# Optimization experiments

Hardware: AMD Instinct MI355X
Metric: run time of the kernel (lower is better)

## Reference

```python
import jax, jax.numpy as jnp
import numpy as np

N, T, F, HID, HEADS, E = 10000, 6, 64, 64, 4, 160000


def gat_conv(x, W, a_src, a_dst, bias, src, dst, n, concat):
    """PyG-style GATConv (self-loops already appended to src/dst).
    x: [n, in]; W: [in, H*C]; a_src/a_dst: [H, C]; returns ([n, H*C] or [n, C], alpha [E', H])."""
    H, C = a_src.shape
    xw = (x @ W).reshape(n, H, C)
    # per-edge unnormalized attention logits
    al = (xw * a_src).sum(-1)[src] + (xw * a_dst).sum(-1)[dst]  # [E', H]
    al = jax.nn.leaky_relu(al, 0.2)
    # segment softmax over destination neighborhoods
    m = jax.ops.segment_max(al, dst, num_segments=n)
    ex = jnp.exp(al - m[dst])
    s = jax.ops.segment_sum(ex, dst, num_segments=n)
    alpha = ex / (s[dst] + 1e-16)
    out = jax.ops.segment_sum(xw[src] * alpha[:, :, None], dst, num_segments=n)  # [n, H, C]
    out = out.reshape(n, H * C) if concat else out.mean(axis=1)
    return out + bias, alpha


def setup_inputs() -> dict:
    key = jax.random.key(0)
    ks = jax.random.split(key, 12)
    sc = 0.05
    return {
        "x": jax.random.normal(ks[0], (N, T, F), jnp.float32),
        "edge_index": jax.random.randint(ks[1], (2, E), 0, N, jnp.int64),
        "W0": jax.random.normal(ks[2], (F, HID), jnp.float32) * sc,
        "a_src0": jax.random.normal(ks[3], (HEADS, HID // HEADS), jnp.float32) * sc,
        "a_dst0": jax.random.normal(ks[4], (HEADS, HID // HEADS), jnp.float32) * sc,
        "b0": jnp.zeros((HID,), jnp.float32),
        "W1": jax.random.normal(ks[5], (HID, HEADS * HID), jnp.float32) * sc,
        "a_src1": jax.random.normal(ks[6], (HEADS, HID), jnp.float32) * sc,
        "a_dst1": jax.random.normal(ks[7], (HEADS, HID), jnp.float32) * sc,
        "b1": jnp.zeros((HID,), jnp.float32),
        "ln_g": jnp.ones((HID,), jnp.float32),
        "ln_b": jnp.zeros((HID,), jnp.float32),
        "W_ih": jax.random.normal(ks[8], (3 * HID, HID), jnp.float32) * sc,
        "W_hh": jax.random.normal(ks[9], (3 * HID, HID), jnp.float32) * sc,
        "b_ih": jnp.zeros((3 * HID,), jnp.float32),
        "b_hh": jnp.zeros((3 * HID,), jnp.float32),
    }


def reference(x, edge_index, W0, a_src0, a_dst0, b0, W1, a_src1, a_dst1, b1,
              ln_g, ln_b, W_ih, W_hh, b_ih, b_hh):
    n = x.shape[0]
    loops = jnp.arange(n)
    src = jnp.concatenate([edge_index[0], loops])  # add self loops
    dst = jnp.concatenate([edge_index[1], loops])

    def gat_step(_, xt):
        h, _a = gat_conv(xt, W0, a_src0, a_dst0, b0, src, dst, n, True)
        h = jax.nn.elu(h)  # dropout is identity in eval mode
        h, alpha = gat_conv(h, W1, a_src1, a_dst1, b1, src, dst, n, False)
        h = jax.nn.elu(h)
        mu = h.mean(-1, keepdims=True)
        v = ((h - mu) ** 2).mean(-1, keepdims=True)
        h = (h - mu) / jnp.sqrt(v + 1e-5) * ln_g + ln_b
        return None, (h, alpha)

    _, (Hs, alphas) = jax.lax.scan(gat_step, None, jnp.moveaxis(x, 1, 0))  # Hs: [T, n, HID]

    def gru_step(h, xt):
        gi = xt @ W_ih.T + b_ih
        gh = h @ W_hh.T + b_hh
        ir, iz, ig = jnp.split(gi, 3, axis=-1)
        hr, hz, hg = jnp.split(gh, 3, axis=-1)
        r = jax.nn.sigmoid(ir + hr)
        z = jax.nn.sigmoid(iz + hz)
        g = jnp.tanh(ig + r * hg)
        return (1.0 - z) * g + z * h, None

    h0 = jnp.zeros((n, W_hh.shape[1]), x.dtype)
    hT, _ = jax.lax.scan(gru_step, h0, Hs)  # last GRU output == last hidden (1 layer)
    attn_edge_index = jnp.stack([src, dst])
    return hT, alphas[-1], attn_edge_index
```

## Files before the change

kernel.cpp:

```cpp
#include <hip/hip_runtime.h>
#include <hip/hip_bf16.h>
#include <cstdint>
#include <cstddef>

#define N_NODES 10000
#define T_STEPS 6
#define F_IN    64
#define HID     64
#define HEADS   4
#define E_EDGES 160000
#define EP      (E_EDGES + N_NODES)
#define TN      (T_STEPS * N_NODES)
#define NTILES  (TN / 16)
#define CAP     96

typedef __hip_bfloat16 bf16;
typedef __attribute__((ext_vector_type(8))) short short8;
typedef __attribute__((ext_vector_type(4))) float floatx4;

__device__ __forceinline__ float bfu(unsigned short s) { return __uint_as_float((unsigned)s << 16); }
__device__ __forceinline__ unsigned short f2bu(float f) {
    bf16 b = __float2bfloat16(f);
    return *(unsigned short*)&b;
}
__device__ __forceinline__ void lds_fence() {
    asm volatile("s_waitcnt lgkmcnt(0)" ::: "memory");
}
__device__ __forceinline__ int xcd_swizzle(int b, int nblk) {
    int q = nblk >> 3, r = nblk & 7;
    int x = b & 7, j = b >> 3;
    return (x < r ? x * (q + 1) : r * (q + 1) + (x - r) * q) + j;
}


__global__ void k_scatter(const int* ei, int* fill,
                          int* csr_src, int* csr_eid, float* out_ei) {
    int e = blockIdx.x * blockDim.x + threadIdx.x;
    if (e >= EP) return;
    int src = (e < E_EDGES) ? ei[e] : (e - E_EDGES);
    int dst = (e < E_EDGES) ? ei[E_EDGES + e] : (e - E_EDGES);
    int pos = atomicAdd(&fill[dst], 1);
    if (pos < CAP) {
        csr_src[dst * CAP + pos] = src;
        csr_eid[dst * CAP + pos] = e;
    }
    out_ei[e] = (float)src;
    out_ei[EP + e] = (float)dst;
}


__global__ __launch_bounds__(256) void k_prep(const float* __restrict__ W0,
                                              const float* __restrict__ W1,
                                              const float* __restrict__ a_src0,
                                              const float* __restrict__ a_dst0,
                                              const float* __restrict__ a_src1,
                                              const float* __restrict__ a_dst1,
                                              const float* __restrict__ W_ih,
                                              const float* __restrict__ W_hh,
                                              bf16* __restrict__ W0bt,
                                              bf16* __restrict__ W1bt,
                                              bf16* __restrict__ wihb,
                                              bf16* __restrict__ whhb,
                                              float* __restrict__ P0s,
                                              float* __restrict__ P0d,
                                              float* __restrict__ P1s,
                                              float* __restrict__ P1d) {
    int b = blockIdx.x, tid = threadIdx.x;
    if (b == 176) {
        int h = tid >> 6, k = tid & 63;
        float ps = 0.f, pd = 0.f;
        for (int c = 0; c < 64; c++) {
            float wv = W1[k * 256 + h * 64 + c];
            ps += wv * a_src1[h * 64 + c];
            pd += wv * a_dst1[h * 64 + c];
        }
        P1s[h * 64 + k] = ps;
        P1d[h * 64 + k] = pd;
        return;
    }
    if (b == 177) {
        int h = tid >> 6, k = tid & 63;
        float ps = 0.f, pd = 0.f;
        for (int c = 0; c < 16; c++) {
            float wv = W0[k * 64 + h * 16 + c];
            ps += wv * a_src0[h * 16 + c];
            pd += wv * a_dst0[h * 16 + c];
        }
        P0s[h * 64 + k] = ps;
        P0d[h * 64 + k] = pd;
        return;
    }
    int i = b * 256 + tid;
    if (i < 4096) {
        W0bt[i] = __float2bfloat16(W0[(i & 63) * 64 + (i >> 6)]);
    } else if (i < 20480) {
        int j = i - 4096; int c = j >> 8, K = j & 255;
        W1bt[j] = __float2bfloat16(W1[(K & 63) * 256 + (K >> 6) * 64 + c]);
    } else if (i < 32768) {
        wihb[i - 20480] = __float2bfloat16(W_ih[i - 20480]);
    } else {
        whhb[i - 32768] = __float2bfloat16(W_hh[i - 32768]);
    }
}

__global__ __launch_bounds__(256) void k_gemm0(const float* __restrict__ x,
                                               const bf16* __restrict__ W0bt,
                                               const float* __restrict__ P0s,
                                               const float* __restrict__ P0d,
                                               bf16* __restrict__ XW0b,
                                               float* __restrict__ ALS0,
                                               float* __restrict__ ALD0) {
    __shared__ __align__(16) bf16 wt[64 * 64];
    int tid = threadIdx.x;
    for (int i = tid; i < 512; i += 256)
        ((short8*)wt)[i] = ((const short8*)W0bt)[i];
    __syncthreads();
    int wv = tid >> 6, lane = tid & 63;
    int tile = blockIdx.x * 4 + wv;
    if (tile >= NTILES) return;
    int rb = tile * 16;
    int m = lane & 15, quad = lane >> 4;
    int row = rb + m;
    int t = row / N_NODES, n = row - t * N_NODES;
    const float* xr = x + ((size_t)n * T_STEPS + t) * F_IN + quad * 8;
    short8 a0, a1;
#pragma unroll
    for (int j = 0; j < 8; j++) {
        a0[j] = (short)f2bu(xr[j]);
        a1[j] = (short)f2bu(xr[32 + j]);
    }
    floatx4 acc[4];
#pragma unroll
    for (int ct = 0; ct < 4; ct++) {
        short8 bb0 = *(const short8*)(wt + (ct * 16 + m) * 64 + quad * 8);
        short8 bb1 = *(const short8*)(wt + (ct * 16 + m) * 64 + 32 + quad * 8);
        floatx4 a = {0.f, 0.f, 0.f, 0.f};
        a = __builtin_amdgcn_mfma_f32_16x16x32_bf16(a0, bb0, a, 0, 0, 0);
        a = __builtin_amdgcn_mfma_f32_16x16x32_bf16(a1, bb1, a, 0, 0, 0);
        acc[ct] = a;
    }
    short8 p0, p1;
#pragma unroll
    for (int j = 0; j < 8; j++) {
        int k0 = quad * 8 + j, k1 = 32 + quad * 8 + j;
        float v0 = 0.f, v1 = 0.f;
        if (m < 4)      { v0 = P0s[m * 64 + k0];       v1 = P0s[m * 64 + k1]; }
        else if (m < 8) { v0 = P0d[(m - 4) * 64 + k0]; v1 = P0d[(m - 4) * 64 + k1]; }
        p0[j] = (short)f2bu(v0);
        p1[j] = (short)f2bu(v1);
    }
    floatx4 ac5 = {0.f, 0.f, 0.f, 0.f};
    ac5 = __builtin_amdgcn_mfma_f32_16x16x32_bf16(a0, p0, ac5, 0, 0, 0);
    ac5 = __builtin_amdgcn_mfma_f32_16x16x32_bf16(a1, p1, ac5, 0, 0, 0);
#pragma unroll
    for (int ct = 0; ct < 4; ct++)
#pragma unroll
        for (int r = 0; r < 4; r++)
            XW0b[(size_t)(rb + quad * 4 + r) * 64 + ct * 16 + m] = __float2bfloat16(acc[ct][r]);
#pragma unroll
    for (int r = 0; r < 4; r++) {
        int orow = rb + quad * 4 + r;
        if (m < 4)      ALS0[orow * 4 + m] = ac5[r];
        else if (m < 8) ALD0[orow * 4 + (m - 4)] = ac5[r];
    }
}

__global__ __launch_bounds__(256) void k_fused0(const int* __restrict__ fill,
                                                const int* __restrict__ csr_src,
                                                const bf16* __restrict__ XW0b,
                                                const float* __restrict__ ALS0,
                                                const float* __restrict__ ALD0,
                                                const float* __restrict__ b0,
                                                const float* __restrict__ P1s,
                                                const float* __restrict__ P1d,
                                                bf16* __restrict__ H0b,
                                                float* __restrict__ ALS1,
                                                float* __restrict__ ALD1) {
    __shared__ unsigned short srcs[4][4][CAP];
    int tid = threadIdx.x;
    int wv = tid >> 6, lane = tid & 63;
    int sub = lane >> 4, il = lane & 15;
    int tile = xcd_swizzle(blockIdx.x, NTILES);
    int wid = tile * 16 + wv * 4 + sub;
    int t = wid / N_NODES, n = wid - t * N_NODES;
    int deg = min(fill[n], CAP);
    int rs = n * CAP;
    int tb = t * N_NODES;
    int hsel = il >> 2;
    float adh = ALD0[(size_t)wid * 4 + hsel];
    for (int idx = il; idx < deg; idx += 16)
        srcs[wv][sub][idx] = (unsigned short)csr_src[rs + idx];
    lds_fence();
    float ssum = 0.f, a0 = 0.f, a1 = 0.f, a2 = 0.f, a3 = 0.f;
    const bf16* hrow = XW0b + (size_t)tb * 64 + il * 4;
    const float* alsb = ALS0 + (size_t)tb * 4 + hsel;
    for (int k = 0; k < deg; k++) {
        int sx = srcs[wv][sub][k];
        float l = alsb[(size_t)sx * 4] + adh;
        l = l > 0.f ? l : 0.2f * l;
        float e = __expf(fminf(l, 80.f));
        ssum += e;
        ushort4 u = *(const ushort4*)(hrow + (size_t)sx * 64);
        a0 += e * bfu(u.x); a1 += e * bfu(u.y);
        a2 += e * bfu(u.z); a3 += e * bfu(u.w);
    }
    float iv = 1.f / (ssum + 1e-16f);
    float4 bv = *(const float4*)(b0 + il * 4);
    float v0 = a0 * iv + bv.x; v0 = v0 > 0.f ? v0 : (__expf(v0) - 1.f);
    float v1 = a1 * iv + bv.y; v1 = v1 > 0.f ? v1 : (__expf(v1) - 1.f);
    float v2 = a2 * iv + bv.z; v2 = v2 > 0.f ? v2 : (__expf(v2) - 1.f);
    float v3 = a3 * iv + bv.w; v3 = v3 > 0.f ? v3 : (__expf(v3) - 1.f);
    ushort4 o4;
    o4.x = f2bu(v0); o4.y = f2bu(v1); o4.z = f2bu(v2); o4.w = f2bu(v3);
    *(ushort4*)(H0b + (size_t)wid * 64 + il * 4) = o4;

    float ps[4], pd[4];
#pragma unroll
    for (int h = 0; h < 4; h++) {
        float4 s4 = *(const float4*)(P1s + h * 64 + il * 4);
        float4 d4 = *(const float4*)(P1d + h * 64 + il * 4);
        ps[h] = v0 * s4.x + v1 * s4.y + v2 * s4.z + v3 * s4.w;
        pd[h] = v0 * d4.x + v1 * d4.y + v2 * d4.z + v3 * d4.w;
    }
#pragma unroll
    for (int o = 1; o <= 8; o <<= 1) {
#pragma unroll
        for (int h = 0; h < 4; h++) {
            ps[h] += __shfl_xor(ps[h], o, 64);
            pd[h] += __shfl_xor(pd[h], o, 64);
        }
    }
    if (il == 0) {
        float4 w1; w1.x = ps[0]; w1.y = ps[1]; w1.z = ps[2]; w1.w = ps[3];
        *(float4*)(ALS1 + (size_t)wid * 4) = w1;
        float4 w2; w2.x = pd[0]; w2.y = pd[1]; w2.z = pd[2]; w2.w = pd[3];
        *(float4*)(ALD1 + (size_t)wid * 4) = w2;
    }
}

__global__ __launch_bounds__(256) void k_fused1(const int* __restrict__ fill,
                                                const int* __restrict__ csr_src,
                                                const int* __restrict__ csr_eid,
                                                const bf16* __restrict__ H0b,
                                                const float* __restrict__ ALS1,
                                                const float* __restrict__ ALD1,
                                                const bf16* __restrict__ W1bt,
                                                const float* __restrict__ b1,
                                                const float* __restrict__ ln_g,
                                                const float* __restrict__ ln_b,
                                                bf16* __restrict__ HSb,
                                                float* __restrict__ out_alpha) {
    __shared__ __align__(16) union SM {
        unsigned short srcs[4][4][CAP];
        struct { bf16 ast[16][264]; float ost[16][68]; } q;
    } sm;
    int tid = threadIdx.x;
    int wv = tid >> 6, lane = tid & 63;
    int sub = lane >> 4, il = lane & 15;
    int tile = xcd_swizzle(blockIdx.x, NTILES);
    int wid = tile * 16 + wv * 4 + sub;
    int t = wid / N_NODES, n = wid - t * N_NODES;
    int deg = min(fill[n], CAP);
    int rs = n * CAP;
    int tb = t * N_NODES;
    bool do_out = (t == T_STEPS - 1);
    int h = il >> 2, q = il & 3;
    float adh = ALD1[(size_t)wid * 4 + h];
    for (int idx = il; idx < deg; idx += 16)
        sm.srcs[wv][sub][idx] = (unsigned short)csr_src[rs + idx];
    lds_fence();
    float ssum = 0.f;
    float acc[16];
#pragma unroll
    for (int j = 0; j < 16; j++) acc[j] = 0.f;
    const bf16* hrow = H0b + (size_t)tb * 64 + q * 16;
    const float* alsb = ALS1 + (size_t)tb * 4 + h;
    for (int k = 0; k < deg; k++) {
        int sx = sm.srcs[wv][sub][k];
        float l = alsb[(size_t)sx * 4] + adh;
        l = l > 0.f ? l : 0.2f * l;
        float e = __expf(fminf(l, 80.f));
        ssum += e;
        const bf16* hp = hrow + (size_t)sx * 64;
        short8 ua = *(const short8*)(hp);
        short8 ub = *(const short8*)(hp + 8);
#pragma unroll
        for (int j = 0; j < 8; j++) {
            acc[j]     += e * bfu((unsigned short)ua[j]);
            acc[8 + j] += e * bfu((unsigned short)ub[j]);
        }
    }
    float iv = 1.f / (ssum + 1e-16f);

    if (do_out) {
        int base = lane & 48;
        float s0 = __shfl(ssum, base | 0,  64);
        float s1 = __shfl(ssum, base | 4,  64);
        float s2 = __shfl(ssum, base | 8,  64);
        float s3 = __shfl(ssum, base | 12, 64);
        float j0 = 1.f / (s0 + 1e-16f), j1 = 1.f / (s1 + 1e-16f);
        float j2 = 1.f / (s2 + 1e-16f), j3 = 1.f / (s3 + 1e-16f);
        float4 ad4 = *(const float4*)(ALD1 + (size_t)wid * 4);
        for (int idx = il; idx < deg; idx += 16) {
            int sx = sm.srcs[wv][sub][idx];
            float4 as = *(const float4*)(ALS1 + (size_t)(tb + sx) * 4);
            float l0 = as.x + ad4.x; l0 = l0 > 0.f ? l0 : 0.2f * l0;
            float l1 = as.y + ad4.y; l1 = l1 > 0.f ? l1 : 0.2f * l1;
            float l2 = as.z + ad4.z; l2 = l2 > 0.f ? l2 : 0.2f * l2;
            float l3 = as.w + ad4.w; l3 = l3 > 0.f ? l3 : 0.2f * l3;
            float4 o4;
            o4.x = __expf(fminf(l0, 80.f)) * j0;
            o4.y = __expf(fminf(l1, 80.f)) * j1;
            o4.z = __expf(fminf(l2, 80.f)) * j2;
            o4.w = __expf(fminf(l3, 80.f)) * j3;
            int eid = csr_eid[rs + idx];
            *(float4*)(out_alpha + (size_t)eid * 4) = o4;
        }
    }

    __syncthreads();
    int r_local = wv * 4 + sub;
    {
        int cb = h * 64 + q * 16;
#pragma unroll
        for (int g4 = 0; g4 < 4; g4++) {
            ushort4 o4;
            o4.x = f2bu(acc[g4 * 4 + 0] * iv);
            o4.y = f2bu(acc[g4 * 4 + 1] * iv);
            o4.z = f2bu(acc[g4 * 4 + 2] * iv);
            o4.w = f2bu(acc[g4 * 4 + 3] * iv);
            *(ushort4*)&sm.q.ast[r_local][cb + g4 * 4] = o4;
        }
    }
    __syncthreads();
    int m = il, quad = sub;
    floatx4 ga = {0.f, 0.f, 0.f, 0.f};
    const bf16* wrow = W1bt + (size_t)(wv * 16 + m) * 256 + quad * 8;
#pragma unroll
    for (int kb = 0; kb < 8; kb++) {
        short8 afk = *(const short8*)&sm.q.ast[m][kb * 32 + quad * 8];
        short8 bfk = *(const short8*)(wrow + kb * 32);
        ga = __builtin_amdgcn_mfma_f32_16x16x32_bf16(afk, bfk, ga, 0, 0, 0);
    }
#pragma unroll
    for (int r = 0; r < 4; r++)
        sm.q.ost[quad * 4 + r][wv * 16 + m] = ga[r];
    __syncthreads();
    int row = wv * 4 + quad;
    float4 vv = *(const float4*)&sm.q.ost[row][m * 4];
    float4 bb = *(const float4*)(b1 + m * 4);
    float v0 = vv.x * 0.25f + bb.x; v0 = v0 > 0.f ? v0 : (__expf(v0) - 1.f);
    float v1 = vv.y * 0.25f + bb.y; v1 = v1 > 0.f ? v1 : (__expf(v1) - 1.f);
    float v2 = vv.z * 0.25f + bb.z; v2 = v2 > 0.f ? v2 : (__expf(v2) - 1.f);
    float v3 = vv.w * 0.25f + bb.w; v3 = v3 > 0.f ? v3 : (__expf(v3) - 1.f);
    float sv = v0 + v1 + v2 + v3;
#pragma unroll
    for (int o = 1; o <= 8; o <<= 1) sv += __shfl_xor(sv, o, 64);
    float mu = sv * (1.f / 64.f);
    float d0 = v0 - mu, d1 = v1 - mu, d2 = v2 - mu, d3 = v3 - mu;
    float qv = d0 * d0 + d1 * d1 + d2 * d2 + d3 * d3;
#pragma unroll
    for (int o = 1; o <= 8; o <<= 1) qv += __shfl_xor(qv, o, 64);
    float rinv = rsqrtf(qv * (1.f / 64.f) + 1e-5f);
    float4 gg = *(const float4*)(ln_g + m * 4);
    float4 lb = *(const float4*)(ln_b + m * 4);
    ushort4 ho;
    ho.x = f2bu(d0 * rinv * gg.x + lb.x);
    ho.y = f2bu(d1 * rinv * gg.y + lb.y);
    ho.z = f2bu(d2 * rinv * gg.z + lb.z);
    ho.w = f2bu(d3 * rinv * gg.w + lb.w);
    *(ushort4*)(HSb + (size_t)(tile * 16 + row) * 64 + m * 4) = ho;
}

__global__ __launch_bounds__(256) void k_gru(const bf16* __restrict__ HSb,
                                             const bf16* __restrict__ wihb,
                                             const float* __restrict__ b_ih,
                                             const bf16* __restrict__ whhb,
                                             const float* __restrict__ b_hh,
                                             float* __restrict__ outh) {
    __shared__ __align__(16) bf16 hbuf[16 * 72];
    int tid = threadIdx.x;
    int wv = tid >> 6, lane = tid & 63;
    int rb = blockIdx.x * 16;
    int m = lane & 15, quad = lane >> 4;
    int fb = wv * 16;
    const int rowR = (fb + m) * 64, rowZ = (64 + fb + m) * 64, rowG = (128 + fb + m) * 64;
    short8 Br0 = *(const short8*)(wihb + rowR + quad * 8);
    short8 Br1 = *(const short8*)(wihb + rowR + 32 + quad * 8);
    short8 Bz0 = *(const short8*)(wihb + rowZ + quad * 8);
    short8 Bz1 = *(const short8*)(wihb + rowZ + 32 + quad * 8);
    short8 Bg0 = *(const short8*)(wihb + rowG + quad * 8);
    short8 Bg1 = *(const short8*)(wihb + rowG + 32 + quad * 8);
    short8 Cr0 = *(const short8*)(whhb + rowR + quad * 8);
    short8 Cr1 = *(const short8*)(whhb + rowR + 32 + quad * 8);
    short8 Cz0 = *(const short8*)(whhb + rowZ + quad * 8);
    short8 Cz1 = *(const short8*)(whhb + rowZ + 32 + quad * 8);
    short8 Cg0 = *(const short8*)(whhb + rowG + quad * 8);
    short8 Cg1 = *(const short8*)(whhb + rowG + 32 + quad * 8);
    float biR = b_ih[fb + m], biZ = b_ih[64 + fb + m], biG = b_ih[128 + fb + m];
    float bhR = b_hh[fb + m], bhZ = b_hh[64 + fb + m], bhG = b_hh[128 + fb + m];
    float hprev[4] = {0.f, 0.f, 0.f, 0.f};

    for (int t = 0; t < T_STEPS; t++) {
        const bf16* xr = HSb + ((size_t)t * N_NODES + rb + m) * 64;
        short8 ax0 = *(const short8*)(xr + quad * 8);
        short8 ax1 = *(const short8*)(xr + 32 + quad * 8);
        short8 ah0, ah1;
        if (t > 0) {
            ah0 = *(const short8*)(hbuf + m * 72 + quad * 8);
            ah1 = *(const short8*)(hbuf + m * 72 + 32 + quad * 8);
        }
        __syncthreads();
        floatx4 aR = {0.f, 0.f, 0.f, 0.f}, aZ = {0.f, 0.f, 0.f, 0.f};
        floatx4 aGi = {0.f, 0.f, 0.f, 0.f}, aGh = {0.f, 0.f, 0.f, 0.f};
        aR = __builtin_amdgcn_mfma_f32_16x16x32_bf16(ax0, Br0, aR, 0, 0, 0);
        aR = __builtin_amdgcn_mfma_f32_16x16x32_bf16(ax1, Br1, aR, 0, 0, 0);
        aZ = __builtin_amdgcn_mfma_f32_16x16x32_bf16(ax0, Bz0, aZ, 0, 0, 0);
        aZ = __builtin_amdgcn_mfma_f32_16x16x32_bf16(ax1, Bz1, aZ, 0, 0, 0);
        aGi = __builtin_amdgcn_mfma_f32_16x16x32_bf16(ax0, Bg0, aGi, 0, 0, 0);
        aGi = __builtin_amdgcn_mfma_f32_16x16x32_bf16(ax1, Bg1, aGi, 0, 0, 0);
        if (t > 0) {
            aR = __builtin_amdgcn_mfma_f32_16x16x32_bf16(ah0, Cr0, aR, 0, 0, 0);
            aR = __builtin_amdgcn_mfma_f32_16x16x32_bf16(ah1, Cr1, aR, 0, 0, 0);
            aZ = __builtin_amdgcn_mfma_f32_16x16x32_bf16(ah0, Cz0, aZ, 0, 0, 0);
            aZ = __builtin_amdgcn_mfma_f32_16x16x32_bf16(ah1, Cz1, aZ, 0, 0, 0);
            aGh = __builtin_amdgcn_mfma_f32_16x16x32_bf16(ah0, Cg0, aGh, 0, 0, 0);
            aGh = __builtin_amdgcn_mfma_f32_16x16x32_bf16(ah1, Cg1, aGh, 0, 0, 0);
        }
#pragma unroll
        for (int r = 0; r < 4; r++) {
            float rr = 1.f / (1.f + __expf(-(aR[r] + biR + bhR)));
            float z  = 1.f / (1.f + __expf(-(aZ[r] + biZ + bhZ)));
            float g  = tanhf(aGi[r] + biG + rr * (aGh[r] + bhG));
            hprev[r] = (1.f - z) * g + z * hprev[r];
        }
        if (t < T_STEPS - 1) {
#pragma unroll
            for (int r = 0; r < 4; r++)
                hbuf[(quad * 4 + r) * 72 + fb + m] = __float2bfloat16(hprev[r]);
            __syncthreads();
        }
    }
#pragma unroll
    for (int r = 0; r < 4; r++)
        outh[(size_t)(rb + quad * 4 + r) * 64 + fb + m] = hprev[r];
}


extern "C" void kernel_launch(void* const* d_in, const int* in_sizes, int n_in,
                              void* d_out, int out_size, void* d_ws, size_t ws_size,
                              hipStream_t stream) {
    const float* x      = (const float*)d_in[0];
    const int*   ei     = (const int*)d_in[1];
    const float* W0     = (const float*)d_in[2];
    const float* a_src0 = (const float*)d_in[3];
    const float* a_dst0 = (const float*)d_in[4];
    const float* b0     = (const float*)d_in[5];
    const float* W1     = (const float*)d_in[6];
    const float* a_src1 = (const float*)d_in[7];
    const float* a_dst1 = (const float*)d_in[8];
    const float* b1     = (const float*)d_in[9];
    const float* ln_g   = (const float*)d_in[10];
    const float* ln_b   = (const float*)d_in[11];
    const float* W_ih   = (const float*)d_in[12];
    const float* W_hh   = (const float*)d_in[13];
    const float* b_ih   = (const float*)d_in[14];
    const float* b_hh   = (const float*)d_in[15];
    float* out = (float*)d_out;

    char* w = (char*)d_ws;
    size_t off = 0;
    auto take = [&](size_t bytes) -> void* {
        void* p = w + off;
        off = (off + bytes + 255) & ~(size_t)255;
        return p;
    };
    int*   fill    = (int*)take(N_NODES * 4);
    int*   csr_src = (int*)take((size_t)N_NODES * CAP * 4);
    int*   csr_eid = (int*)take((size_t)N_NODES * CAP * 4);
    bf16*  XW0b    = (bf16*)take((size_t)TN * 64 * 2);
    float* ALS0    = (float*)take((size_t)TN * 4 * 4);
    float* ALD0    = (float*)take((size_t)TN * 4 * 4);
    bf16*  H0b     = (bf16*)take((size_t)TN * 64 * 2);
    float* P0s     = (float*)take(256 * 4);
    float* P0d     = (float*)take(256 * 4);
    float* P1s     = (float*)take(256 * 4);
    float* P1d     = (float*)take(256 * 4);
    float* ALS1    = (float*)take((size_t)TN * 4 * 4);
    float* ALD1    = (float*)take((size_t)TN * 4 * 4);
    bf16*  HSb     = (bf16*)take((size_t)TN * 64 * 2);
    bf16*  W0bt    = (bf16*)take(4096 * 2);
    bf16*  W1bt    = (bf16*)take(16384 * 2);
    bf16*  wihb    = (bf16*)take(12288 * 2);
    bf16*  whhb    = (bf16*)take(12288 * 2);
    (void)ws_size; (void)in_sizes; (void)n_in; (void)out_size;

    const int B = 256;
    float* out_ei = out + (size_t)N_NODES * HID + (size_t)EP * HEADS;

    hipMemsetAsync(fill, 0, N_NODES * 4, stream);
    k_prep<<<178, B, 0, stream>>>(W0, W1, a_src0, a_dst0, a_src1, a_dst1, W_ih, W_hh,
                                  W0bt, W1bt, wihb, whhb, P0s, P0d, P1s, P1d);
    k_scatter<<<(EP + B - 1) / B, B, 0, stream>>>(ei, fill, csr_src, csr_eid, out_ei);

    const int GT = (NTILES + 3) / 4;
    k_gemm0<<<GT, B, 0, stream>>>(x, W0bt, P0s, P0d, XW0b, ALS0, ALD0);
    k_fused0<<<NTILES, B, 0, stream>>>(fill, csr_src, XW0b, ALS0, ALD0, b0,
                                       P1s, P1d, H0b, ALS1, ALD1);

    k_fused1<<<NTILES, B, 0, stream>>>(fill, csr_src, csr_eid, H0b, ALS1, ALD1,
                                       W1bt, b1, ln_g, ln_b, HSb,
                                       out + (size_t)N_NODES * HID);

    k_gru<<<N_NODES / 16, B, 0, stream>>>(HSb, wihb, b_ih, whhb, b_hh, out);
}
```

Measured before the change: 211.2 us.

## Remap layer-1 aggregation lanes to channels and use int transposed LDS source lists

```diff
diff --git a/kernel.cpp b/kernel.cpp
--- a/kernel.cpp
+++ b/kernel.cpp
@@ -176,12 +176,13 @@
                                                 bf16* __restrict__ H0b,
                                                 float* __restrict__ ALS1,
                                                 float* __restrict__ ALD1) {
-    __shared__ unsigned short srcs[4][4][CAP];
+    __shared__ int srcs[CAP][16];
     int tid = threadIdx.x;
     int wv = tid >> 6, lane = tid & 63;
     int sub = lane >> 4, il = lane & 15;
+    int g = wv * 4 + sub;
     int tile = xcd_swizzle(blockIdx.x, NTILES);
-    int wid = tile * 16 + wv * 4 + sub;
+    int wid = tile * 16 + g;
     int t = wid / N_NODES, n = wid - t * N_NODES;
     int deg = min(fill[n], CAP);
     int rs = n * CAP;
@@ -189,13 +190,13 @@
     int hsel = il >> 2;
     float adh = ALD0[(size_t)wid * 4 + hsel];
     for (int idx = il; idx < deg; idx += 16)
-        srcs[wv][sub][idx] = (unsigned short)csr_src[rs + idx];
+        srcs[idx][g] = csr_src[rs + idx];
     lds_fence();
     float ssum = 0.f, a0 = 0.f, a1 = 0.f, a2 = 0.f, a3 = 0.f;
     const bf16* hrow = XW0b + (size_t)tb * 64 + il * 4;
     const float* alsb = ALS0 + (size_t)tb * 4 + hsel;
     for (int k = 0; k < deg; k++) {
-        int sx = srcs[wv][sub][k];
+        int sx = srcs[k][g];
         float l = alsb[(size_t)sx * 4] + adh;
         l = l > 0.f ? l : 0.2f * l;
         float e = __expf(fminf(l, 80.f));
@@ -251,86 +252,82 @@
                                                 bf16* __restrict__ HSb,
                                                 float* __restrict__ out_alpha) {
     __shared__ __align__(16) union SM {
-        unsigned short srcs[4][4][CAP];
+        int srcs[CAP][16];
         struct { bf16 ast[16][264]; float ost[16][68]; } q;
     } sm;
     int tid = threadIdx.x;
     int wv = tid >> 6, lane = tid & 63;
     int sub = lane >> 4, il = lane & 15;
+    int g = wv * 4 + sub;
     int tile = xcd_swizzle(blockIdx.x, NTILES);
-    int wid = tile * 16 + wv * 4 + sub;
+    int wid = tile * 16 + g;
     int t = wid / N_NODES, n = wid - t * N_NODES;
     int deg = min(fill[n], CAP);
     int rs = n * CAP;
     int tb = t * N_NODES;
     bool do_out = (t == T_STEPS - 1);
-    int h = il >> 2, q = il & 3;
-    float adh = ALD1[(size_t)wid * 4 + h];
+    float4 ad4 = *(const float4*)(ALD1 + (size_t)wid * 4);
     for (int idx = il; idx < deg; idx += 16)
-        sm.srcs[wv][sub][idx] = (unsigned short)csr_src[rs + idx];
+        sm.srcs[idx][g] = csr_src[rs + idx];
     lds_fence();
-    float ssum = 0.f;
-    float acc[16];
-#pragma unroll
-    for (int j = 0; j < 16; j++) acc[j] = 0.f;
-    const bf16* hrow = H0b + (size_t)tb * 64 + q * 16;
-    const float* alsb = ALS1 + (size_t)tb * 4 + h;
+    float s0 = 0.f, s1 = 0.f, s2 = 0.f, s3 = 0.f;
+    float acc[4][4];
+#pragma unroll
+    for (int h = 0; h < 4; h++)
+#pragma unroll
+        for (int j = 0; j < 4; j++) acc[h][j] = 0.f;
+    const bf16* hrow = H0b + (size_t)tb * 64 + il * 4;
+    const float* alsb = ALS1 + (size_t)tb * 4;
     for (int k = 0; k < deg; k++) {
-        int sx = sm.srcs[wv][sub][k];
-        float l = alsb[(size_t)sx * 4] + adh;
-        l = l > 0.f ? l : 0.2f * l;
-        float e = __expf(fminf(l, 80.f));
-        ssum += e;
-        const bf16* hp = hrow + (size_t)sx * 64;
-        short8 ua = *(const short8*)(hp);
-        short8 ub = *(const short8*)(hp + 8);
-#pragma unroll
-        for (int j = 0; j < 8; j++) {
-            acc[j]     += e * bfu((unsigned short)ua[j]);
-            acc[8 + j] += e * bfu((unsigned short)ub[j]);
-        }
-    }
-    float iv = 1.f / (ssum + 1e-16f);
+        int sx = sm.srcs[k][g];
+        float4 as = *(const float4*)(alsb + (size_t)sx * 4);
+        float l0 = as.x + ad4.x; l0 = l0 > 0.f ? l0 : 0.2f * l0;
+        float l1 = as.y + ad4.y; l1 = l1 > 0.f ? l1 : 0.2f * l1;
+        float l2 = as.z + ad4.z; l2 = l2 > 0.f ? l2 : 0.2f * l2;
+        float l3 = as.w + ad4.w; l3 = l3 > 0.f ? l3 : 0.2f * l3;
+        float e0 = __expf(fminf(l0, 80.f));
+        float e1 = __expf(fminf(l1, 80.f));
+        float e2 = __expf(fminf(l2, 80.f));
+        float e3 = __expf(fminf(l3, 80.f));
+        s0 += e0; s1 += e1; s2 += e2; s3 += e3;
+        ushort4 u = *(const ushort4*)(hrow + (size_t)sx * 64);
+        float x0 = bfu(u.x), x1 = bfu(u.y), x2 = bfu(u.z), x3 = bfu(u.w);
+        acc[0][0] += e0 * x0; acc[0][1] += e0 * x1; acc[0][2] += e0 * x2; acc[0][3] += e0 * x3;
+        acc[1][0] += e1 * x0; acc[1][1] += e1 * x1; acc[1][2] += e1 * x2; acc[1][3] += e1 * x3;
+        acc[2][0] += e2 * x0; acc[2][1] += e2 * x1; acc[2][2] += e2 * x2; acc[2][3] += e2 * x3;
+        acc[3][0] += e3 * x0; acc[3][1] += e3 * x1; acc[3][2] += e3 * x2; acc[3][3] += e3 * x3;
+    }
+    float iv0 = 1.f / (s0 + 1e-16f), iv1 = 1.f / (s1 + 1e-16f);
+    float iv2 = 1.f / (s2 + 1e-16f), iv3 = 1.f / (s3 + 1e-16f);
 
     if (do_out) {
-        int base = lane & 48;
-        float s0 = __shfl(ssum, base | 0,  64);
-        float s1 = __shfl(ssum, base | 4,  64);
-        float s2 = __shfl(ssum, base | 8,  64);
-        float s3 = __shfl(ssum, base | 12, 64);
-        float j0 = 1.f / (s0 + 1e-16f), j1 = 1.f / (s1 + 1e-16f);
-        float j2 = 1.f / (s2 + 1e-16f), j3 = 1.f / (s3 + 1e-16f);
-        float4 ad4 = *(const float4*)(ALD1 + (size_t)wid * 4);
         for (int idx = il; idx < deg; idx += 16) {
-            int sx = sm.srcs[wv][sub][idx];
-            float4 as = *(const float4*)(ALS1 + (size_t)(tb + sx) * 4);
+            int sx = sm.srcs[idx][g];
+            float4 as = *(const float4*)(alsb + (size_t)sx * 4);
             float l0 = as.x + ad4.x; l0 = l0 > 0.f ? l0 : 0.2f * l0;
             float l1 = as.y + ad4.y; l1 = l1 > 0.f ? l1 : 0.2f * l1;
             float l2 = as.z + ad4.z; l2 = l2 > 0.f ? l2 : 0.2f * l2;
             float l3 = as.w + ad4.w; l3 = l3 > 0.f ? l3 : 0.2f * l3;
             float4 o4;
-            o4.x = __expf(fminf(l0, 80.f)) * j0;
-            o4.y = __expf(fminf(l1, 80.f)) * j1;
-            o4.z = __expf(fminf(l2, 80.f)) * j2;
-            o4.w = __expf(fminf(l3, 80.f)) * j3;
+            o4.x = __expf(fminf(l0, 80.f)) * iv0;
+            o4.y = __expf(fminf(l1, 80.f)) * iv1;
+            o4.z = __expf(fminf(l2, 80.f)) * iv2;
+            o4.w = __expf(fminf(l3, 80.f)) * iv3;
             int eid = csr_eid[rs + idx];
             *(float4*)(out_alpha + (size_t)eid * 4) = o4;
         }
     }
 
     __syncthreads();
-    int r_local = wv * 4 + sub;
-    {
-        int cb = h * 64 + q * 16;
-#pragma unroll
-        for (int g4 = 0; g4 < 4; g4++) {
-            ushort4 o4;
-            o4.x = f2bu(acc[g4 * 4 + 0] * iv);
-            o4.y = f2bu(acc[g4 * 4 + 1] * iv);
-            o4.z = f2bu(acc[g4 * 4 + 2] * iv);
-            o4.w = f2bu(acc[g4 * 4 + 3] * iv);
-            *(ushort4*)&sm.q.ast[r_local][cb + g4 * 4] = o4;
-        }
+    float ivh[4] = { iv0, iv1, iv2, iv3 };
+#pragma unroll
+    for (int h = 0; h < 4; h++) {
+        ushort4 o4;
+        o4.x = f2bu(acc[h][0] * ivh[h]);
+        o4.y = f2bu(acc[h][1] * ivh[h]);
+        o4.z = f2bu(acc[h][2] * ivh[h]);
+        o4.w = f2bu(acc[h][3] * ivh[h]);
+        *(ushort4*)&sm.q.ast[g][h * 64 + il * 4] = o4;
     }
     __syncthreads();
     int m = il, quad = sub;
```

Result: no change. 212.4 us (+0.6%).
